# Performance work log

Hardware: AMD Instinct MI355X
Metric: run time of the kernel (lower is better)

Reference implementation:

```python
import jax, jax.numpy as jnp
import numpy as np

NEIGH_RADIUS = 1
NEIGH_DILATION = 1
NB_ITER = 3
GROUP_NB = 4
SOFTMAX_FACT = 1.0
EPS = 1e-8


def _directions():
    # matches computeNeighborsCoord: (x, y) pairs, row-major over y then x, center removed
    r = NEIGH_RADIUS
    return [(x * NEIGH_DILATION, y * NEIGH_DILATION)
            for y in range(-r, r + 1) for x in range(-r, r + 1)
            if not (x == 0 and y == 0)]


def _shift(feat, dx, dy):
    # out[..., i, j] = feat[..., i+dy, j+dx], zero outside the image; mask marks valid positions
    H, W = feat.shape[2], feat.shape[3]
    shifted = jnp.roll(feat, shift=(-dy, -dx), axis=(2, 3))
    vy = (np.arange(H) + dy >= 0) & (np.arange(H) + dy < H)
    vx = (np.arange(W) + dx >= 0) & (np.arange(W) + dx < W)
    mask = jnp.asarray(np.outer(vy, vx).astype(np.float32))[None, None]  # [1,1,H,W]
    return shifted * mask, mask


def _cossim(a, b):
    # channel-wise cosine similarity -> [B,1,H,W]
    num = jnp.sum(a * b, axis=1, keepdims=True)
    den = jnp.sqrt(jnp.sum(a * a, axis=1, keepdims=True)) * jnp.sqrt(jnp.sum(b * b, axis=1, keepdims=True))
    return num / jnp.maximum(den, EPS)


def _total_sim(feat, dirs):
    # mask-normalized mean cosine similarity with the 8 neighbors -> [B,1,H,W]
    num = 0.0
    cnt = 0.0
    for dx, dy in dirs:
        fs, m = _shift(feat, dx, dy)
        num = num + _cossim(feat, fs) * m
        cnt = cnt + m
    return num / cnt


def setup_inputs() -> dict:
    key = jax.random.key(0)
    features = jax.random.normal(key, (8, 32, 256, 256), dtype=jnp.float32)
    return {"features": features}


def reference(features):
    dirs = _directions()
    sim_maps = [_total_sim(features, dirs)]
    for _ in range(NB_ITER):
        sims = []
        fshifts = []
        for dx, dy in dirs:
            fs, m = _shift(features, dx, dy)
            sims.append(_cossim(features, fs) * m)  # masked sim, zeros at invalid positions
            fshifts.append(fs)                       # already masked shift
        all_sim = jax.nn.softmax(SOFTMAX_FACT * jnp.concatenate(sims, axis=1), axis=1)  # [B,8,H,W]
        new_feat = sum(all_sim[:, i:i + 1] * fshifts[i] for i in range(len(dirs)))       # [B,C,H,W]
        sim_maps.append(_total_sim(features, dirs))  # NOTE: pre-update features, as in original
        new_feat = new_feat / jnp.sum(all_sim, axis=1, keepdims=True)  # == conv2d with ones(1,8,1,1)
        features = new_feat
    out = jnp.concatenate(sim_maps, axis=1)  # [B, nbIter+1, H, W]
    B, T, H, W = out.shape
    out = out.reshape(B // GROUP_NB, GROUP_NB, T, H, W).mean(axis=1)
    return out
```

## Files before the change

### kernel.cpp

```cpp
#include <hip/hip_runtime.h>

#define HH 256
#define WW 256
#define CC 32
#define HWSZ (HH * WW)
#define IMGSZ (CC * HWSZ)
#define NIMG 8
#define EPSV 1e-8f
#define NCH (CC / 2)

__device__ __forceinline__ void acc_pass1(const float v[3][6],
                                          float sq[3][6], float dotv[8][4])
{
#pragma unroll
    for (int r = 0; r < 3; ++r)
#pragma unroll
        for (int j = 0; j < 6; ++j) sq[r][j] = fmaf(v[r][j], v[r][j], sq[r][j]);
    int d = 0;
#pragma unroll
    for (int dyi = 0; dyi < 3; ++dyi)
#pragma unroll
        for (int dxi = 0; dxi < 3; ++dxi) {
            if (dyi == 1 && dxi == 1) continue;
#pragma unroll
            for (int i = 0; i < 4; ++i)
                dotv[d][i] = fmaf(v[1][i + 1], v[dyi][i + dxi], dotv[d][i]);
            ++d;
        }
}

__device__ __forceinline__ void acc_pass2(const float v[3][6],
                                          const float w[8][4], float o[4])
{
    int d = 0;
#pragma unroll
    for (int dyi = 0; dyi < 3; ++dyi)
#pragma unroll
        for (int dxi = 0; dxi < 3; ++dxi) {
            if (dyi == 1 && dxi == 1) continue;
#pragma unroll
            for (int i = 0; i < 4; ++i)
                o[i] = fmaf(w[d][i], v[dyi][i + dxi], o[i]);
            ++d;
        }
}

__device__ __forceinline__ void gload16(const void* g, void* l)
{
    __builtin_amdgcn_global_load_lds(
        (const __attribute__((address_space(1))) void*)g,
        (__attribute__((address_space(3))) void*)l, 16, 0, 0);
}

#define STAGE(SLOT) { \
    const int ch_ = (SLOT) & 15; \
    const int bo_ = ((SLOT) & 3) * 8192; \
    gload16(gsrc0 + (size_t)ch_ * HWSZ,        ldst0 + bo_); \
    gload16(gsrc0 + (size_t)(ch_ + 16) * HWSZ, ldst0 + bo_ + 4096); }

#define WAITB(VM) { asm volatile("s_waitcnt vmcnt(" #VM ")" ::: "memory"); \
                    __builtin_amdgcn_s_barrier(); }

#define LOADV(G, VV) { \
    const char* sp_ = slabb + ((G) & 3) * 8192; \
    _Pragma("unroll") \
    for (int r_ = 0; r_ < 3; ++r_) { \
        float4 m_ = *(const float4*)(sp_ + bM + r_ * 1024); \
        float e_ = 0.f; \
        if (edge) e_ = *(const float*)(sp_ + bE + r_ * 1024); \
        const float lu_ = __shfl_up(m_.w, 1); \
        const float rd_ = __shfl_down(m_.x, 1); \
        const bool ok_ = rowok[r_]; \
        VV[r_][0] = (ok_ && xl) ? ((tx == 0)  ? e_ : lu_) : 0.f; \
        VV[r_][1] = ok_ ? m_.x : 0.f; \
        VV[r_][2] = ok_ ? m_.y : 0.f; \
        VV[r_][3] = ok_ ? m_.z : 0.f; \
        VV[r_][4] = ok_ ? m_.w : 0.f; \
        VV[r_][5] = (ok_ && xr) ? ((tx == 31) ? e_ : rd_) : 0.f; \
    } }

template <bool YEDGE, bool COMPUTE_NEXT>
__device__ __forceinline__ void step_body(const float* __restrict__ F,
                                          float* __restrict__ Fn,
                                          float* __restrict__ simout,
                                          char* slabb, int b, int rowblk, int tid)
{
    const int wave = tid >> 6;
    const int lane = tid & 63;
    const int half = lane >> 5;
    const int tx   = lane & 31;
    const int y0   = rowblk * 2;
    const int y    = y0 + (wave >> 1);
    const int x0   = (wave & 1) * 128 + (tx << 2);
    const int c0   = half * NCH;

    const bool ym = YEDGE ? (y > 0) : true;
    const bool yp = YEDGE ? (y < HH - 1) : true;
    const bool xl = x0 > 0, xr = x0 < WW - 4;
    const bool rowok[3] = { ym, true, yp };
    const bool colok[6] = { xl, true, true, true, true, xr };

    const float* Fb = F + (size_t)b * IMGSZ;

    int arow = y0 - 1 + wave;
    if (YEDGE) arow = arow < 0 ? 0 : (arow > HH - 1 ? HH - 1 : arow);
    const float* gsrc0 = Fb + arow * WW + (lane << 2);
    char* ldst0 = slabb + wave * 1024;

    const int rbase = half * 4096 + (wave >> 1) * 1024;
    const int bM = rbase + x0 * 4;
    const int bL = rbase + (xl ? x0 * 4 - 4 : 0);
    const int bR = rbase + (xr ? x0 * 4 + 16 : 1020);
    const bool edge = (tx == 0) || (tx == 31);
    const int bE = (tx == 31) ? bR : bL;

    float sq[3][6];
    float dotv[8][4];
#pragma unroll
    for (int r = 0; r < 3; ++r)
#pragma unroll
        for (int j = 0; j < 6; ++j) sq[r][j] = 0.f;
#pragma unroll
    for (int d = 0; d < 8; ++d)
#pragma unroll
        for (int i = 0; i < 4; ++i) dotv[d][i] = 0.f;

    STAGE(0) STAGE(1) STAGE(2)

#pragma unroll 1
    for (int g = 0; g < (COMPUTE_NEXT ? 16 : 13); ++g) {
        WAITB(4)
        STAGE(g + 3)
        float v[3][6];
        LOADV(g, v)
        acc_pass1(v, sq, dotv);
    }
    if (!COMPUTE_NEXT) {
        { WAITB(4) float v[3][6]; LOADV(13, v) acc_pass1(v, sq, dotv); }
        { WAITB(2) float v[3][6]; LOADV(14, v) acc_pass1(v, sq, dotv); }
        { WAITB(0) float v[3][6]; LOADV(15, v) acc_pass1(v, sq, dotv); }
    }

#pragma unroll
    for (int r = 0; r < 3; ++r)
#pragma unroll
        for (int j = 0; j < 6; ++j) sq[r][j] += __shfl_xor(sq[r][j], 32);
#pragma unroll
    for (int d = 0; d < 8; ++d)
#pragma unroll
        for (int i = 0; i < 4; ++i) dotv[d][i] += __shfl_xor(dotv[d][i], 32);

    float nrm[3][6];
#pragma unroll
    for (int r = 0; r < 3; ++r)
#pragma unroll
        for (int j = 0; j < 6; ++j) nrm[r][j] = __builtin_amdgcn_sqrtf(sq[r][j]);

    float w[8][4];
    float simarr[4];
#pragma unroll
    for (int i = 0; i < 4; ++i) {
        float s[8];
        const float cn = nrm[1][i + 1];
        float tot = 0.f, cnt = 0.f;
        int d = 0;
#pragma unroll
        for (int dyi = 0; dyi < 3; ++dyi)
#pragma unroll
            for (int dxi = 0; dxi < 3; ++dxi) {
                if (dyi == 1 && dxi == 1) continue;
                const bool m = rowok[dyi] && colok[i + dxi];
                const float den = fmaxf(cn * nrm[dyi][i + dxi], EPSV);
                const float cs = dotv[d][i] * __builtin_amdgcn_rcpf(den);
                s[d] = m ? cs : 0.f;
                tot += s[d];
                cnt += m ? 1.f : 0.f;
                ++d;
            }
        simarr[i] = tot * __builtin_amdgcn_rcpf(cnt);
        if (COMPUTE_NEXT) {
            float mx = s[0];
#pragma unroll
            for (int d2 = 1; d2 < 8; ++d2) mx = fmaxf(mx, s[d2]);
            float wsum = 0.f;
#pragma unroll
            for (int d2 = 0; d2 < 8; ++d2) { w[d2][i] = __expf(s[d2] - mx); wsum += w[d2][i]; }
            const float inv = __builtin_amdgcn_rcpf(wsum);
#pragma unroll
            for (int d2 = 0; d2 < 8; ++d2) w[d2][i] *= inv;
        }
    }
    if (half == 0) {
        float4 simv = { simarr[0], simarr[1], simarr[2], simarr[3] };
        *reinterpret_cast<float4*>(simout + b * HWSZ + y * WW + x0) = simv;
    }

    if (COMPUTE_NEXT) {
        float* outp = Fn + (size_t)b * IMGSZ + (size_t)c0 * HWSZ + y * WW + x0;
#pragma unroll 1
        for (int g = 16; g < 29; ++g) {
            WAITB(4)
            STAGE(g + 3)
            float v[3][6];
            LOADV(g, v)
            float o[4] = { 0.f, 0.f, 0.f, 0.f };
            acc_pass2(v, w, o);
            float4 ov = { o[0], o[1], o[2], o[3] };
            *reinterpret_cast<float4*>(outp + (g & 15) * HWSZ) = ov;
        }
        { WAITB(4) float v[3][6]; LOADV(29, v)
          float o[4] = { 0.f, 0.f, 0.f, 0.f }; acc_pass2(v, w, o);
          float4 ov = { o[0], o[1], o[2], o[3] };
          *reinterpret_cast<float4*>(outp + 13 * HWSZ) = ov; }
        { WAITB(2) float v[3][6]; LOADV(30, v)
          float o[4] = { 0.f, 0.f, 0.f, 0.f }; acc_pass2(v, w, o);
          float4 ov = { o[0], o[1], o[2], o[3] };
          *reinterpret_cast<float4*>(outp + 14 * HWSZ) = ov; }
        { WAITB(0) float v[3][6]; LOADV(31, v)
          float o[4] = { 0.f, 0.f, 0.f, 0.f }; acc_pass2(v, w, o);
          float4 ov = { o[0], o[1], o[2], o[3] };
          *reinterpret_cast<float4*>(outp + 15 * HWSZ) = ov; }
    }
}

template <bool COMPUTE_NEXT>
__global__ __launch_bounds__(256, 4) void step_kernel(const float* __restrict__ F,
                                                      float* __restrict__ Fn,
                                                      float* __restrict__ simout)
{
    const int linear = blockIdx.y * (HH / 2) + blockIdx.x;
    const int remap  = (linear & 7) * 128 + (linear >> 3);
    const int b      = remap >> 7;
    const int rowblk = remap & 127;

    __shared__ float4 slab4[2048];

    if (rowblk != 0 && rowblk != 127)
        step_body<false, COMPUTE_NEXT>(F, Fn, simout, (char*)slab4, b, rowblk, threadIdx.x);
    else
        step_body<true,  COMPUTE_NEXT>(F, Fn, simout, (char*)slab4, b, rowblk, threadIdx.x);
}

__global__ __launch_bounds__(256) void reduce_kernel(const float* __restrict__ sims,
                                                     float* __restrict__ out)
{
    const int idx = blockIdx.x * blockDim.x + threadIdx.x;
    const int p4 = idx & (HWSZ / 4 - 1);
    const int t  = (idx >> 14) & 3;
    const int g  = idx >> 16;
    const int tt = (t <= 1) ? 0 : (t - 1);
    const float4* s = reinterpret_cast<const float4*>(sims) +
                      (size_t)(tt * NIMG + g * 4) * (HWSZ / 4) + p4;
    float4 a = s[0];
    float4 b = s[HWSZ / 4];
    float4 c = s[2 * (HWSZ / 4)];
    float4 d = s[3 * (HWSZ / 4)];
    float4 o;
    o.x = 0.25f * (a.x + b.x + c.x + d.x);
    o.y = 0.25f * (a.y + b.y + c.y + d.y);
    o.z = 0.25f * (a.z + b.z + c.z + d.z);
    o.w = 0.25f * (a.w + b.w + c.w + d.w);
    reinterpret_cast<float4*>(out)[idx] = o;
}

extern "C" void kernel_launch(void* const* d_in, const int* in_sizes, int n_in,
                              void* d_out, int out_size, void* d_ws, size_t ws_size,
                              hipStream_t stream)
{
    const float* F0 = (const float*)d_in[0];
    float* F1   = (float*)d_ws;
    float* F2   = F1 + (size_t)NIMG * IMGSZ;
    float* sims = F2 + (size_t)NIMG * IMGSZ;

    dim3 block(256);
    dim3 grid(HH / 2, NIMG);

    hipLaunchKernelGGL((step_kernel<true>),  grid, block, 0, stream, F0, F1, sims);
    hipLaunchKernelGGL((step_kernel<true>),  grid, block, 0, stream, F1, F2, sims + (size_t)NIMG * HWSZ);
    hipLaunchKernelGGL((step_kernel<false>), grid, block, 0, stream, F2, nullptr, sims + (size_t)2 * NIMG * HWSZ);

    hipLaunchKernelGGL(reduce_kernel, dim3((2 * 4 * HWSZ / 4) / 256), block, 0, stream,
                       sims, (float*)d_out);
}
```

Before: 102.7 us.

## Restructure LDS staging pipeline to two channel-pairs per barrier with triple buffering

The async global-to-LDS pipeline now moves two channel pairs per stage into three 16 KB buffers instead of one pair into four 8 KB slots. Each barrier therefore covers two channels of compute, halving the number of waitcnt/barrier synchronisations per block. LDS per block grows from 32 KB to 48 KB and the launch-bounds occupancy hint drops from 4 to 3 blocks per CU, so fewer waves are available to hide latency. The loads for the next stage are issued after the compute rather than before it, which changes how much prefetch depth is in flight.

```diff
diff --git a/kernel.cpp b/kernel.cpp
--- a/kernel.cpp
+++ b/kernel.cpp
@@ -52,17 +52,17 @@
         (__attribute__((address_space(3))) void*)l, 16, 0, 0);
 }
 
-#define STAGE(SLOT) { \
-    const int ch_ = (SLOT) & 15; \
-    const int bo_ = ((SLOT) & 3) * 8192; \
-    gload16(gsrc0 + (size_t)ch_ * HWSZ,        ldst0 + bo_); \
-    gload16(gsrc0 + (size_t)(ch_ + 16) * HWSZ, ldst0 + bo_ + 4096); }
+#define STAGE2(POFF, CH0) { \
+    gload16(gsrc0 + (size_t)(CH0) * HWSZ,        ldst0 + (POFF)); \
+    gload16(gsrc0 + (size_t)((CH0) + 16) * HWSZ, ldst0 + (POFF) + 4096); \
+    gload16(gsrc0 + (size_t)((CH0) + 1) * HWSZ,  ldst0 + (POFF) + 8192); \
+    gload16(gsrc0 + (size_t)((CH0) + 17) * HWSZ, ldst0 + (POFF) + 12288); }
 
 #define WAITB(VM) { asm volatile("s_waitcnt vmcnt(" #VM ")" ::: "memory"); \
                     __builtin_amdgcn_s_barrier(); }
 
-#define LOADV(G, VV) { \
-    const char* sp_ = slabb + ((G) & 3) * 8192; \
+#define LOADV(OFFB, VV) { \
+    const char* sp_ = slabb + (OFFB); \
     _Pragma("unroll") \
     for (int r_ = 0; r_ < 3; ++r_) { \
         float4 m_ = *(const float4*)(sp_ + bM + r_ * 1024); \
@@ -79,6 +79,8 @@
         VV[r_][5] = (ok_ && xr) ? ((tx == 31) ? e_ : rd_) : 0.f; \
     } }
 
+#define ROT3(P) { P = (P == 2) ? 0 : P + 1; }
+
 template <bool YEDGE, bool COMPUTE_NEXT>
 __device__ __forceinline__ void step_body(const float* __restrict__ F,
                                           float* __restrict__ Fn,
@@ -125,20 +127,26 @@
 #pragma unroll
         for (int i = 0; i < 4; ++i) dotv[d][i] = 0.f;
 
-    STAGE(0) STAGE(1) STAGE(2)
+    STAGE2(0, 0) STAGE2(16384, 2)
+    int po = 0;
 
 #pragma unroll 1
-    for (int g = 0; g < (COMPUTE_NEXT ? 16 : 13); ++g) {
+    for (int k = 0; k < (COMPUTE_NEXT ? 8 : 6); ++k) {
+        const int qo = (po == 0) ? 2 : po - 1;
         WAITB(4)
-        STAGE(g + 3)
         float v[3][6];
-        LOADV(g, v)
-        acc_pass1(v, sq, dotv);
+        LOADV(po * 16384, v)        acc_pass1(v, sq, dotv);
+        LOADV(po * 16384 + 8192, v) acc_pass1(v, sq, dotv);
+        STAGE2(qo * 16384, (2 * k + 4) & 15)
+        ROT3(po)
     }
     if (!COMPUTE_NEXT) {
-        { WAITB(4) float v[3][6]; LOADV(13, v) acc_pass1(v, sq, dotv); }
-        { WAITB(2) float v[3][6]; LOADV(14, v) acc_pass1(v, sq, dotv); }
-        { WAITB(0) float v[3][6]; LOADV(15, v) acc_pass1(v, sq, dotv); }
+        { WAITB(4) float v[3][6];
+          LOADV(po * 16384, v)        acc_pass1(v, sq, dotv);
+          LOADV(po * 16384 + 8192, v) acc_pass1(v, sq, dotv); ROT3(po) }
+        { WAITB(0) float v[3][6];
+          LOADV(po * 16384, v)        acc_pass1(v, sq, dotv);
+          LOADV(po * 16384 + 8192, v) acc_pass1(v, sq, dotv); }
     }
 
 #pragma unroll
@@ -197,34 +205,38 @@
 
     if (COMPUTE_NEXT) {
         float* outp = Fn + (size_t)b * IMGSZ + (size_t)c0 * HWSZ + y * WW + x0;
+
+#define PASS2_CH(OFFB, CH) { \
+            float v[3][6]; LOADV(OFFB, v) \
+            float o[4] = { 0.f, 0.f, 0.f, 0.f }; acc_pass2(v, w, o); \
+            float4 ov = { o[0], o[1], o[2], o[3] }; \
+            *reinterpret_cast<float4*>(outp + (CH) * HWSZ) = ov; }
+
+        { const int qo = (po == 0) ? 2 : po - 1;
+          WAITB(5)
+          PASS2_CH(po * 16384, 0) PASS2_CH(po * 16384 + 8192, 1)
+          STAGE2(qo * 16384, 4)
+          ROT3(po) }
 #pragma unroll 1
-        for (int g = 16; g < 29; ++g) {
-            WAITB(4)
-            STAGE(g + 3)
-            float v[3][6];
-            LOADV(g, v)
-            float o[4] = { 0.f, 0.f, 0.f, 0.f };
-            acc_pass2(v, w, o);
-            float4 ov = { o[0], o[1], o[2], o[3] };
-            *reinterpret_cast<float4*>(outp + (g & 15) * HWSZ) = ov;
-        }
-        { WAITB(4) float v[3][6]; LOADV(29, v)
-          float o[4] = { 0.f, 0.f, 0.f, 0.f }; acc_pass2(v, w, o);
-          float4 ov = { o[0], o[1], o[2], o[3] };
-          *reinterpret_cast<float4*>(outp + 13 * HWSZ) = ov; }
-        { WAITB(2) float v[3][6]; LOADV(30, v)
-          float o[4] = { 0.f, 0.f, 0.f, 0.f }; acc_pass2(v, w, o);
-          float4 ov = { o[0], o[1], o[2], o[3] };
-          *reinterpret_cast<float4*>(outp + 14 * HWSZ) = ov; }
-        { WAITB(0) float v[3][6]; LOADV(31, v)
-          float o[4] = { 0.f, 0.f, 0.f, 0.f }; acc_pass2(v, w, o);
-          float4 ov = { o[0], o[1], o[2], o[3] };
-          *reinterpret_cast<float4*>(outp + 15 * HWSZ) = ov; }
+        for (int k = 9; k < 14; ++k) {
+            const int qo = (po == 0) ? 2 : po - 1;
+            WAITB(6)
+            const int ch = 2 * (k - 8);
+            PASS2_CH(po * 16384, ch) PASS2_CH(po * 16384 + 8192, ch + 1)
+            STAGE2(qo * 16384, (2 * k + 4) & 15)
+            ROT3(po)
+        }
+        { WAITB(6)
+          PASS2_CH(po * 16384, 12) PASS2_CH(po * 16384 + 8192, 13)
+          ROT3(po) }
+        { WAITB(2)
+          PASS2_CH(po * 16384, 14) PASS2_CH(po * 16384 + 8192, 15) }
+#undef PASS2_CH
     }
 }
 
 template <bool COMPUTE_NEXT>
-__global__ __launch_bounds__(256, 4) void step_kernel(const float* __restrict__ F,
+__global__ __launch_bounds__(256, 3) void step_kernel(const float* __restrict__ F,
                                                       float* __restrict__ Fn,
                                                       float* __restrict__ simout)
 {
@@ -233,7 +245,7 @@
     const int b      = remap >> 7;
     const int rowblk = remap & 127;
 
-    __shared__ float4 slab4[2048];
+    __shared__ float4 slab4[3072];
 
     if (rowblk != 0 && rowblk != 127)
         step_body<false, COMPUTE_NEXT>(F, Fn, simout, (char*)slab4, b, rowblk, threadIdx.x);
```

Result: slower. 108.8 us (+6.0%).

## Deduplicate horizontal dot products and halo norms via shuffles and LDS exchange

Applied to the files above, without the earlier changes.

The channel-accumulation pass stops computing the left/right neighbor dot products per pixel. It keeps one running product per adjacent pixel pair instead, and accumulates squared norms only for the 4 owned pixels. Halo norms are fetched from adjacent lanes with shuffles, and across the wave boundary through a small shared exchange array behind a barrier. This cuts FMAs and accumulator registers in the hot loop, possibly raising occupancy, at the cost of an extra barrier and a few shuffles after the reduction.

```diff
diff --git a/kernel.cpp b/kernel.cpp
--- a/kernel.cpp
+++ b/kernel.cpp
@@ -10,23 +10,26 @@
 #define NCH (CC / 2)
 
 __device__ __forceinline__ void acc_pass1(const float v[3][6],
-                                          float sq[3][6], float dotv[8][4])
+                                          float sqc[3][4], float dirs[6][4],
+                                          float ew[5])
 {
 #pragma unroll
     for (int r = 0; r < 3; ++r)
 #pragma unroll
-        for (int j = 0; j < 6; ++j) sq[r][j] = fmaf(v[r][j], v[r][j], sq[r][j]);
-    int d = 0;
-#pragma unroll
-    for (int dyi = 0; dyi < 3; ++dyi)
-#pragma unroll
-        for (int dxi = 0; dxi < 3; ++dxi) {
-            if (dyi == 1 && dxi == 1) continue;
-#pragma unroll
-            for (int i = 0; i < 4; ++i)
-                dotv[d][i] = fmaf(v[1][i + 1], v[dyi][i + dxi], dotv[d][i]);
-            ++d;
-        }
+        for (int j = 0; j < 4; ++j)
+            sqc[r][j] = fmaf(v[r][j + 1], v[r][j + 1], sqc[r][j]);
+#pragma unroll
+    for (int i = 0; i < 4; ++i) {
+        const float c = v[1][i + 1];
+        dirs[0][i] = fmaf(c, v[0][i],     dirs[0][i]);
+        dirs[1][i] = fmaf(c, v[0][i + 1], dirs[1][i]);
+        dirs[2][i] = fmaf(c, v[0][i + 2], dirs[2][i]);
+        dirs[3][i] = fmaf(c, v[2][i],     dirs[3][i]);
+        dirs[4][i] = fmaf(c, v[2][i + 1], dirs[4][i]);
+        dirs[5][i] = fmaf(c, v[2][i + 2], dirs[5][i]);
+    }
+#pragma unroll
+    for (int j = 0; j < 5; ++j) ew[j] = fmaf(v[1][j], v[1][j + 1], ew[j]);
 }
 
 __device__ __forceinline__ void acc_pass2(const float v[3][6],
@@ -83,7 +86,8 @@
 __device__ __forceinline__ void step_body(const float* __restrict__ F,
                                           float* __restrict__ Fn,
                                           float* __restrict__ simout,
-                                          char* slabb, int b, int rowblk, int tid)
+                                          char* slabb, float* exch,
+                                          int b, int rowblk, int tid)
 {
     const int wave = tid >> 6;
     const int lane = tid & 63;
@@ -114,16 +118,19 @@
     const bool edge = (tx == 0) || (tx == 31);
     const int bE = (tx == 31) ? bR : bL;
 
-    float sq[3][6];
-    float dotv[8][4];
+    float sqc[3][4];
+    float dirs[6][4];
+    float ew[5];
 #pragma unroll
     for (int r = 0; r < 3; ++r)
 #pragma unroll
-        for (int j = 0; j < 6; ++j) sq[r][j] = 0.f;
-#pragma unroll
-    for (int d = 0; d < 8; ++d)
-#pragma unroll
-        for (int i = 0; i < 4; ++i) dotv[d][i] = 0.f;
+        for (int j = 0; j < 4; ++j) sqc[r][j] = 0.f;
+#pragma unroll
+    for (int d = 0; d < 6; ++d)
+#pragma unroll
+        for (int i = 0; i < 4; ++i) dirs[d][i] = 0.f;
+#pragma unroll
+    for (int j = 0; j < 5; ++j) ew[j] = 0.f;
 
     STAGE(0) STAGE(1) STAGE(2)
 
@@ -133,33 +140,65 @@
         STAGE(g + 3)
         float v[3][6];
         LOADV(g, v)
-        acc_pass1(v, sq, dotv);
+        acc_pass1(v, sqc, dirs, ew);
     }
     if (!COMPUTE_NEXT) {
-        { WAITB(4) float v[3][6]; LOADV(13, v) acc_pass1(v, sq, dotv); }
-        { WAITB(2) float v[3][6]; LOADV(14, v) acc_pass1(v, sq, dotv); }
-        { WAITB(0) float v[3][6]; LOADV(15, v) acc_pass1(v, sq, dotv); }
+        { WAITB(4) float v[3][6]; LOADV(13, v) acc_pass1(v, sqc, dirs, ew); }
+        { WAITB(2) float v[3][6]; LOADV(14, v) acc_pass1(v, sqc, dirs, ew); }
+        { WAITB(0) float v[3][6]; LOADV(15, v) acc_pass1(v, sqc, dirs, ew); }
     }
 
 #pragma unroll
     for (int r = 0; r < 3; ++r)
 #pragma unroll
-        for (int j = 0; j < 6; ++j) sq[r][j] += __shfl_xor(sq[r][j], 32);
-#pragma unroll
-    for (int d = 0; d < 8; ++d)
-#pragma unroll
-        for (int i = 0; i < 4; ++i) dotv[d][i] += __shfl_xor(dotv[d][i], 32);
+        for (int j = 0; j < 4; ++j) sqc[r][j] += __shfl_xor(sqc[r][j], 32);
+#pragma unroll
+    for (int d = 0; d < 6; ++d)
+#pragma unroll
+        for (int i = 0; i < 4; ++i) dirs[d][i] += __shfl_xor(dirs[d][i], 32);
+#pragma unroll
+    for (int j = 0; j < 5; ++j) ew[j] += __shfl_xor(ew[j], 32);
+
+    if (half == 0 && tx == ((wave & 1) ? 0 : 31)) {
+#pragma unroll
+        for (int r = 0; r < 3; ++r)
+            exch[(wave >> 1) * 6 + (wave & 1) * 3 + r] =
+                (wave & 1) ? sqc[r][0] : sqc[r][3];
+    }
+    asm volatile("s_waitcnt lgkmcnt(0)" ::: "memory");
+    __builtin_amdgcn_s_barrier();
+
+    float sqh0[3], sqh5[3];
+#pragma unroll
+    for (int r = 0; r < 3; ++r) {
+        sqh0[r] = __shfl_up(sqc[r][3], 1);
+        sqh5[r] = __shfl_down(sqc[r][0], 1);
+    }
+    if (tx == 31 && (wave & 1) == 0) {
+#pragma unroll
+        for (int r = 0; r < 3; ++r) sqh5[r] = exch[(wave >> 1) * 6 + 3 + r];
+    }
+    if (tx == 0 && (wave & 1) == 1) {
+#pragma unroll
+        for (int r = 0; r < 3; ++r) sqh0[r] = exch[(wave >> 1) * 6 + r];
+    }
 
     float nrm[3][6];
 #pragma unroll
-    for (int r = 0; r < 3; ++r)
-#pragma unroll
-        for (int j = 0; j < 6; ++j) nrm[r][j] = __builtin_amdgcn_sqrtf(sq[r][j]);
+    for (int r = 0; r < 3; ++r) {
+        nrm[r][0] = __builtin_amdgcn_sqrtf(sqh0[r]);
+#pragma unroll
+        for (int j = 0; j < 4; ++j) nrm[r][j + 1] = __builtin_amdgcn_sqrtf(sqc[r][j]);
+        nrm[r][5] = __builtin_amdgcn_sqrtf(sqh5[r]);
+    }
 
     float w[8][4];
     float simarr[4];
 #pragma unroll
     for (int i = 0; i < 4; ++i) {
+        const float num[8] = { dirs[0][i], dirs[1][i], dirs[2][i],
+                               ew[i], ew[i + 1],
+                               dirs[3][i], dirs[4][i], dirs[5][i] };
         float s[8];
         const float cn = nrm[1][i + 1];
         float tot = 0.f, cnt = 0.f;
@@ -171,7 +210,7 @@
                 if (dyi == 1 && dxi == 1) continue;
                 const bool m = rowok[dyi] && colok[i + dxi];
                 const float den = fmaxf(cn * nrm[dyi][i + dxi], EPSV);
-                const float cs = dotv[d][i] * __builtin_amdgcn_rcpf(den);
+                const float cs = num[d] * __builtin_amdgcn_rcpf(den);
                 s[d] = m ? cs : 0.f;
                 tot += s[d];
                 cnt += m ? 1.f : 0.f;
@@ -234,11 +273,12 @@
     const int rowblk = remap & 127;
 
     __shared__ float4 slab4[2048];
+    __shared__ float exch[12];
 
     if (rowblk != 0 && rowblk != 127)
-        step_body<false, COMPUTE_NEXT>(F, Fn, simout, (char*)slab4, b, rowblk, threadIdx.x);
+        step_body<false, COMPUTE_NEXT>(F, Fn, simout, (char*)slab4, exch, b, rowblk, threadIdx.x);
     else
-        step_body<true,  COMPUTE_NEXT>(F, Fn, simout, (char*)slab4, b, rowblk, threadIdx.x);
+        step_body<true,  COMPUTE_NEXT>(F, Fn, simout, (char*)slab4, exch, b, rowblk, threadIdx.x);
 }
 
 __global__ __launch_bounds__(256) void reduce_kernel(const float* __restrict__ sims,
```

Measured after the change: 104.2 us. Within noise of the previous version (+1.5%).

## Store intermediate feature maps in fp16 to halve memory traffic

Applied to the files above, without the earlier changes.

The intermediate feature tensors F1 and F2 are now written and read as fp16 instead of fp32. The first step kernel reads fp32 input and emits packed half outputs. The later steps use a new half-precision staging path with a smaller LDS slab and retuned wait counts, converting to fp32 for the arithmetic. The aim is to cut the DRAM bytes of these memory-bound passes, at the cost of reduced precision in the intermediate features, which may affect accuracy tolerances.

```diff
diff --git a/kernel.cpp b/kernel.cpp
--- a/kernel.cpp
+++ b/kernel.cpp
@@ -1,4 +1,5 @@
 #include <hip/hip_runtime.h>
+#include <hip/hip_fp16.h>
 
 #define HH 256
 #define WW 256
@@ -52,14 +53,25 @@
         (__attribute__((address_space(3))) void*)l, 16, 0, 0);
 }
 
+__device__ __forceinline__ float cvtlo(unsigned u)
+{ return __half2float(__ushort_as_half((unsigned short)(u & 0xffffu))); }
+__device__ __forceinline__ float cvthi(unsigned u)
+{ return __half2float(__ushort_as_half((unsigned short)(u >> 16))); }
+__device__ __forceinline__ unsigned pkh(float a, float b)
+{
+    return (unsigned)__half_as_ushort(__float2half_rn(a)) |
+           ((unsigned)__half_as_ushort(__float2half_rn(b)) << 16);
+}
+
+#define WAITB(VM) { asm volatile("s_waitcnt vmcnt(" #VM ")" ::: "memory"); \
+                    __builtin_amdgcn_s_barrier(); }
+
+
 #define STAGE(SLOT) { \
     const int ch_ = (SLOT) & 15; \
     const int bo_ = ((SLOT) & 3) * 8192; \
     gload16(gsrc0 + (size_t)ch_ * HWSZ,        ldst0 + bo_); \
     gload16(gsrc0 + (size_t)(ch_ + 16) * HWSZ, ldst0 + bo_ + 4096); }
-
-#define WAITB(VM) { asm volatile("s_waitcnt vmcnt(" #VM ")" ::: "memory"); \
-                    __builtin_amdgcn_s_barrier(); }
 
 #define LOADV(G, VV) { \
     const char* sp_ = slabb + ((G) & 3) * 8192; \
@@ -79,11 +91,11 @@
         VV[r_][5] = (ok_ && xr) ? ((tx == 31) ? e_ : rd_) : 0.f; \
     } }
 
-template <bool YEDGE, bool COMPUTE_NEXT>
-__device__ __forceinline__ void step_body(const float* __restrict__ F,
-                                          float* __restrict__ Fn,
-                                          float* __restrict__ simout,
-                                          char* slabb, int b, int rowblk, int tid)
+template <bool YEDGE>
+__device__ __forceinline__ void step1_body(const float* __restrict__ F,
+                                           unsigned short* __restrict__ Fn,
+                                           float* __restrict__ simout,
+                                           char* slabb, int b, int rowblk, int tid)
 {
     const int wave = tid >> 6;
     const int lane = tid & 63;
@@ -101,7 +113,6 @@
     const bool colok[6] = { xl, true, true, true, true, xr };
 
     const float* Fb = F + (size_t)b * IMGSZ;
-
     int arow = y0 - 1 + wave;
     if (YEDGE) arow = arow < 0 ? 0 : (arow > HH - 1 ? HH - 1 : arow);
     const float* gsrc0 = Fb + arow * WW + (lane << 2);
@@ -128,17 +139,203 @@
     STAGE(0) STAGE(1) STAGE(2)
 
 #pragma unroll 1
-    for (int g = 0; g < (COMPUTE_NEXT ? 16 : 13); ++g) {
+    for (int g = 0; g < 16; ++g) {
         WAITB(4)
         STAGE(g + 3)
         float v[3][6];
         LOADV(g, v)
         acc_pass1(v, sq, dotv);
     }
+
+#pragma unroll
+    for (int r = 0; r < 3; ++r)
+#pragma unroll
+        for (int j = 0; j < 6; ++j) sq[r][j] += __shfl_xor(sq[r][j], 32);
+#pragma unroll
+    for (int d = 0; d < 8; ++d)
+#pragma unroll
+        for (int i = 0; i < 4; ++i) dotv[d][i] += __shfl_xor(dotv[d][i], 32);
+
+    float nrm[3][6];
+#pragma unroll
+    for (int r = 0; r < 3; ++r)
+#pragma unroll
+        for (int j = 0; j < 6; ++j) nrm[r][j] = __builtin_amdgcn_sqrtf(sq[r][j]);
+
+    float w[8][4];
+    float simarr[4];
+#pragma unroll
+    for (int i = 0; i < 4; ++i) {
+        float s[8];
+        const float cn = nrm[1][i + 1];
+        float tot = 0.f, cnt = 0.f;
+        int d = 0;
+#pragma unroll
+        for (int dyi = 0; dyi < 3; ++dyi)
+#pragma unroll
+            for (int dxi = 0; dxi < 3; ++dxi) {
+                if (dyi == 1 && dxi == 1) continue;
+                const bool m = rowok[dyi] && colok[i + dxi];
+                const float den = fmaxf(cn * nrm[dyi][i + dxi], EPSV);
+                const float cs = dotv[d][i] * __builtin_amdgcn_rcpf(den);
+                s[d] = m ? cs : 0.f;
+                tot += s[d];
+                cnt += m ? 1.f : 0.f;
+                ++d;
+            }
+        simarr[i] = tot * __builtin_amdgcn_rcpf(cnt);
+        {
+            float mx = s[0];
+#pragma unroll
+            for (int d2 = 1; d2 < 8; ++d2) mx = fmaxf(mx, s[d2]);
+            float wsum = 0.f;
+#pragma unroll
+            for (int d2 = 0; d2 < 8; ++d2) { w[d2][i] = __expf(s[d2] - mx); wsum += w[d2][i]; }
+            const float inv = __builtin_amdgcn_rcpf(wsum);
+#pragma unroll
+            for (int d2 = 0; d2 < 8; ++d2) w[d2][i] *= inv;
+        }
+    }
+    if (half == 0) {
+        float4 simv = { simarr[0], simarr[1], simarr[2], simarr[3] };
+        *reinterpret_cast<float4*>(simout + b * HWSZ + y * WW + x0) = simv;
+    }
+
+    {
+        unsigned short* outp = Fn + (size_t)b * IMGSZ + (size_t)c0 * HWSZ + y * WW + x0;
+#pragma unroll 1
+        for (int g = 16; g < 29; ++g) {
+            WAITB(4)
+            STAGE(g + 3)
+            float v[3][6];
+            LOADV(g, v)
+            float o[4] = { 0.f, 0.f, 0.f, 0.f };
+            acc_pass2(v, w, o);
+            uint2 ov; ov.x = pkh(o[0], o[1]); ov.y = pkh(o[2], o[3]);
+            *reinterpret_cast<uint2*>(outp + (g & 15) * HWSZ) = ov;
+        }
+        { WAITB(4) float v[3][6]; LOADV(29, v)
+          float o[4] = { 0.f, 0.f, 0.f, 0.f }; acc_pass2(v, w, o);
+          uint2 ov; ov.x = pkh(o[0], o[1]); ov.y = pkh(o[2], o[3]);
+          *reinterpret_cast<uint2*>(outp + 13 * HWSZ) = ov; }
+        { WAITB(2) float v[3][6]; LOADV(30, v)
+          float o[4] = { 0.f, 0.f, 0.f, 0.f }; acc_pass2(v, w, o);
+          uint2 ov; ov.x = pkh(o[0], o[1]); ov.y = pkh(o[2], o[3]);
+          *reinterpret_cast<uint2*>(outp + 14 * HWSZ) = ov; }
+        { WAITB(0) float v[3][6]; LOADV(31, v)
+          float o[4] = { 0.f, 0.f, 0.f, 0.f }; acc_pass2(v, w, o);
+          uint2 ov; ov.x = pkh(o[0], o[1]); ov.y = pkh(o[2], o[3]);
+          *reinterpret_cast<uint2*>(outp + 15 * HWSZ) = ov; }
+    }
+}
+
+__global__ __launch_bounds__(256, 4) void step1_kernel(const float* __restrict__ F,
+                                                       unsigned short* __restrict__ Fn,
+                                                       float* __restrict__ simout)
+{
+    const int linear = blockIdx.y * (HH / 2) + blockIdx.x;
+    const int remap  = (linear & 7) * 128 + (linear >> 3);
+    const int b      = remap >> 7;
+    const int rowblk = remap & 127;
+
+    __shared__ float4 slab4[2048];
+
+    if (rowblk != 0 && rowblk != 127)
+        step1_body<false>(F, Fn, simout, (char*)slab4, b, rowblk, threadIdx.x);
+    else
+        step1_body<true>(F, Fn, simout, (char*)slab4, b, rowblk, threadIdx.x);
+}
+
+
+#define STAGE_H(SLOT) { \
+    gload16(gsrcH + (size_t)(((SLOT) & 15) + halfS * 16) * HWSZ, \
+            ldstH + ((SLOT) & 3) * 4096); }
+
+#define LOADV_H(G, VV) { \
+    const char* sp_ = slabb + ((G) & 3) * 4096; \
+    _Pragma("unroll") \
+    for (int r_ = 0; r_ < 3; ++r_) { \
+        uint2 b_ = *(const uint2*)(sp_ + bMH + r_ * 512); \
+        float e_ = 0.f; \
+        if (edge && eok) { \
+            unsigned eu_ = *(const unsigned*)(sp_ + bEH + r_ * 512); \
+            e_ = (tx == 31) ? cvtlo(eu_) : cvthi(eu_); \
+        } \
+        const unsigned lu32_ = __shfl_up(b_.y, 1); \
+        const unsigned rd32_ = __shfl_down(b_.x, 1); \
+        const bool ok_ = rowok[r_]; \
+        VV[r_][0] = (ok_ && xl) ? ((tx == 0)  ? e_ : cvthi(lu32_)) : 0.f; \
+        VV[r_][1] = ok_ ? cvtlo(b_.x) : 0.f; \
+        VV[r_][2] = ok_ ? cvthi(b_.x) : 0.f; \
+        VV[r_][3] = ok_ ? cvtlo(b_.y) : 0.f; \
+        VV[r_][4] = ok_ ? cvthi(b_.y) : 0.f; \
+        VV[r_][5] = (ok_ && xr) ? ((tx == 31) ? e_ : cvtlo(rd32_)) : 0.f; \
+    } }
+
+template <bool YEDGE, bool COMPUTE_NEXT>
+__device__ __forceinline__ void steph_body(const unsigned short* __restrict__ F,
+                                           unsigned short* __restrict__ Fn,
+                                           float* __restrict__ simout,
+                                           char* slabb, int b, int rowblk, int tid)
+{
+    const int wave = tid >> 6;
+    const int lane = tid & 63;
+    const int half = lane >> 5;
+    const int tx   = lane & 31;
+    const int y0   = rowblk * 2;
+    const int y    = y0 + (wave >> 1);
+    const int x0   = (wave & 1) * 128 + (tx << 2);
+    const int c0   = half * NCH;
+
+    const bool ym = YEDGE ? (y > 0) : true;
+    const bool yp = YEDGE ? (y < HH - 1) : true;
+    const bool xl = x0 > 0, xr = x0 < WW - 4;
+    const bool rowok[3] = { ym, true, yp };
+    const bool colok[6] = { xl, true, true, true, true, xr };
+
+    const unsigned short* Fb = F + (size_t)b * IMGSZ;
+
+    const int halfS = wave >> 1;
+    const int rp    = wave & 1;
+    int srow = y0 - 1 + 2 * rp;
+    int dsh  = 0;
+    if (YEDGE) {
+        if (srow < 0)            { srow = 0;      dsh = 512;  }
+        else if (srow + 1 > HH - 1) { srow = HH - 2; dsh = -512; }
+    }
+    const unsigned short* gsrcH = Fb + srow * WW + lane * 8;
+    char* ldstH = slabb + halfS * 2048 + rp * 1024 + dsh;
+
+    const int bMH = half * 2048 + (wave >> 1) * 512 + x0 * 2;
+    const bool edge = (tx == 0) || (tx == 31);
+    const bool eok  = (tx == 31) ? xr : xl;
+    const int bEH   = (tx == 31) ? (bMH + 8) : (bMH - 4);
+
+    float sq[3][6];
+    float dotv[8][4];
+#pragma unroll
+    for (int r = 0; r < 3; ++r)
+#pragma unroll
+        for (int j = 0; j < 6; ++j) sq[r][j] = 0.f;
+#pragma unroll
+    for (int d = 0; d < 8; ++d)
+#pragma unroll
+        for (int i = 0; i < 4; ++i) dotv[d][i] = 0.f;
+
+    STAGE_H(0) STAGE_H(1) STAGE_H(2)
+
+#pragma unroll 1
+    for (int g = 0; g < (COMPUTE_NEXT ? 16 : 13); ++g) {
+        WAITB(2)
+        STAGE_H(g + 3)
+        float v[3][6];
+        LOADV_H(g, v)
+        acc_pass1(v, sq, dotv);
+    }
     if (!COMPUTE_NEXT) {
-        { WAITB(4) float v[3][6]; LOADV(13, v) acc_pass1(v, sq, dotv); }
-        { WAITB(2) float v[3][6]; LOADV(14, v) acc_pass1(v, sq, dotv); }
-        { WAITB(0) float v[3][6]; LOADV(15, v) acc_pass1(v, sq, dotv); }
+        { WAITB(2) float v[3][6]; LOADV_H(13, v) acc_pass1(v, sq, dotv); }
+        { WAITB(1) float v[3][6]; LOADV_H(14, v) acc_pass1(v, sq, dotv); }
+        { WAITB(0) float v[3][6]; LOADV_H(15, v) acc_pass1(v, sq, dotv); }
     }
 
 #pragma unroll
@@ -196,49 +393,47 @@
     }
 
     if (COMPUTE_NEXT) {
-        float* outp = Fn + (size_t)b * IMGSZ + (size_t)c0 * HWSZ + y * WW + x0;
+        unsigned short* outp = Fn + (size_t)b * IMGSZ + (size_t)c0 * HWSZ + y * WW + x0;
+
+#define PASS2H(VM, G) { \
+            WAITB(VM) \
+            if ((G) < 29) STAGE_H((G) + 3) \
+            float v[3][6]; \
+            LOADV_H(G, v) \
+            float o[4] = { 0.f, 0.f, 0.f, 0.f }; \
+            acc_pass2(v, w, o); \
+            uint2 ov; ov.x = pkh(o[0], o[1]); ov.y = pkh(o[2], o[3]); \
+            *reinterpret_cast<uint2*>(outp + ((G) & 15) * HWSZ) = ov; }
+
+        PASS2H(3, 16)
+        PASS2H(4, 17)
 #pragma unroll 1
-        for (int g = 16; g < 29; ++g) {
-            WAITB(4)
-            STAGE(g + 3)
-            float v[3][6];
-            LOADV(g, v)
-            float o[4] = { 0.f, 0.f, 0.f, 0.f };
-            acc_pass2(v, w, o);
-            float4 ov = { o[0], o[1], o[2], o[3] };
-            *reinterpret_cast<float4*>(outp + (g & 15) * HWSZ) = ov;
-        }
-        { WAITB(4) float v[3][6]; LOADV(29, v)
-          float o[4] = { 0.f, 0.f, 0.f, 0.f }; acc_pass2(v, w, o);
-          float4 ov = { o[0], o[1], o[2], o[3] };
-          *reinterpret_cast<float4*>(outp + 13 * HWSZ) = ov; }
-        { WAITB(2) float v[3][6]; LOADV(30, v)
-          float o[4] = { 0.f, 0.f, 0.f, 0.f }; acc_pass2(v, w, o);
-          float4 ov = { o[0], o[1], o[2], o[3] };
-          *reinterpret_cast<float4*>(outp + 14 * HWSZ) = ov; }
-        { WAITB(0) float v[3][6]; LOADV(31, v)
-          float o[4] = { 0.f, 0.f, 0.f, 0.f }; acc_pass2(v, w, o);
-          float4 ov = { o[0], o[1], o[2], o[3] };
-          *reinterpret_cast<float4*>(outp + 15 * HWSZ) = ov; }
+        for (int g = 18; g < 29; ++g) {
+            PASS2H(5, g)
+        }
+        PASS2H(5, 29)
+        PASS2H(4, 30)
+        PASS2H(3, 31)
+#undef PASS2H
     }
 }
 
 template <bool COMPUTE_NEXT>
-__global__ __launch_bounds__(256, 4) void step_kernel(const float* __restrict__ F,
-                                                      float* __restrict__ Fn,
-                                                      float* __restrict__ simout)
+__global__ __launch_bounds__(256, 4) void steph_kernel(const unsigned short* __restrict__ F,
+                                                       unsigned short* __restrict__ Fn,
+                                                       float* __restrict__ simout)
 {
     const int linear = blockIdx.y * (HH / 2) + blockIdx.x;
     const int remap  = (linear & 7) * 128 + (linear >> 3);
     const int b      = remap >> 7;
     const int rowblk = remap & 127;
 
-    __shared__ float4 slab4[2048];
+    __shared__ float4 slabH[1024];
 
     if (rowblk != 0 && rowblk != 127)
-        step_body<false, COMPUTE_NEXT>(F, Fn, simout, (char*)slab4, b, rowblk, threadIdx.x);
+        steph_body<false, COMPUTE_NEXT>(F, Fn, simout, (char*)slabH, b, rowblk, threadIdx.x);
     else
-        step_body<true,  COMPUTE_NEXT>(F, Fn, simout, (char*)slab4, b, rowblk, threadIdx.x);
+        steph_body<true,  COMPUTE_NEXT>(F, Fn, simout, (char*)slabH, b, rowblk, threadIdx.x);
 }
 
 __global__ __launch_bounds__(256) void reduce_kernel(const float* __restrict__ sims,
@@ -268,16 +463,16 @@
                               hipStream_t stream)
 {
     const float* F0 = (const float*)d_in[0];
-    float* F1   = (float*)d_ws;
-    float* F2   = F1 + (size_t)NIMG * IMGSZ;
-    float* sims = F2 + (size_t)NIMG * IMGSZ;
+    unsigned short* F1h = (unsigned short*)d_ws;
+    unsigned short* F2h = F1h + (size_t)NIMG * IMGSZ;
+    float* sims = (float*)(F2h + (size_t)NIMG * IMGSZ);
 
     dim3 block(256);
     dim3 grid(HH / 2, NIMG);
 
-    hipLaunchKernelGGL((step_kernel<true>),  grid, block, 0, stream, F0, F1, sims);
-    hipLaunchKernelGGL((step_kernel<true>),  grid, block, 0, stream, F1, F2, sims + (size_t)NIMG * HWSZ);
-    hipLaunchKernelGGL((step_kernel<false>), grid, block, 0, stream, F2, nullptr, sims + (size_t)2 * NIMG * HWSZ);
+    hipLaunchKernelGGL(step1_kernel,          grid, block, 0, stream, F0, F1h, sims);
+    hipLaunchKernelGGL((steph_kernel<true>),  grid, block, 0, stream, F1h, F2h, sims + (size_t)NIMG * HWSZ);
+    hipLaunchKernelGGL((steph_kernel<false>), grid, block, 0, stream, F2h, nullptr, sims + (size_t)2 * NIMG * HWSZ);
 
     hipLaunchKernelGGL(reduce_kernel, dim3((2 * 4 * HWSZ / 4) / 256), block, 0, stream,
                        sims, (float*)d_out);
```

New measurement: 98.96 us. 1.04x faster.
